# Optimization experiments

Measured on AMD Instinct MI355X. Metric: run time of the kernel, lower is better.

## Reference

```python
import jax, jax.numpy as jnp
import numpy as np

N_NODES = 100000
N_EDGES = 1600000
K = 10          # APPNP propagation steps
ALPHA = 0.1     # teleport probability


def appnp_propagate(src, dst, h):
    """DGL APPNPConv (eval mode, no edge dropout): symmetric-normalized
    k-step personalized-pagerank propagation over the edge list."""
    n = h.shape[0]
    deg = jax.ops.segment_sum(jnp.ones_like(dst, dtype=h.dtype), dst, num_segments=n)
    norm = jnp.clip(deg, 1.0, None) ** -0.5  # [N]
    h0 = h
    for _ in range(K):
        msg = (h * norm[:, None])[src]                      # [E, D] gather
        agg = jax.ops.segment_sum(msg, dst, num_segments=n) # [N, D] scatter-add
        h = (1.0 - ALPHA) * agg * norm[:, None] + ALPHA * h0
    return h


def setup_inputs() -> dict:
    key = jax.random.key(0)
    ks = jax.random.split(key, 7)
    input_dim, hidden, classes = 256, 48, 16
    features = jax.random.normal(ks[0], (N_NODES, input_dim), dtype=jnp.float32)
    src = jax.random.randint(ks[1], (N_EDGES,), 0, N_NODES, dtype=jnp.int32)
    dst = jax.random.randint(ks[2], (N_EDGES,), 0, N_NODES, dtype=jnp.int32)
    # xavier_normal-ish init for fc weights
    W1 = jax.random.normal(ks[3], (hidden, input_dim), dtype=jnp.float32) * (2.0 / (hidden + input_dim)) ** 0.5
    b1 = jnp.zeros((hidden,), dtype=jnp.float32)
    W2 = jax.random.normal(ks[4], (classes, hidden), dtype=jnp.float32) * (2.0 / (classes + hidden)) ** 0.5
    b2 = jnp.zeros((classes,), dtype=jnp.float32)
    return {"features": features, "src": src, "dst": dst,
            "W1": W1, "b1": b1, "W2": W2, "b2": b2}


def reference(features, src, dst, W1, b1, W2, b2):
    # fc1
    h = features @ W1.T + b1              # [N, hidden]
    # layer1: APPNP propagation
    x = appnp_propagate(src, dst, h)
    # fc2 + elu
    x = jax.nn.elu(x @ W2.T + b2)         # [N, classes]
    # layer2: APPNP propagation
    x = appnp_propagate(src, dst, x)
    return jax.nn.elu(x)
```

## Files before the change

### kernel.cpp

```cpp
#include <hip/hip_runtime.h>
#include <hip/hip_fp16.h>
#include <math.h>

#define IN_DIM 256
#define HID 48
#define CLS 16
#define K_STEPS 10
#define ALPHA 0.1f


__global__ void zero_int_kernel(int* __restrict__ p, int n) {
    int i = blockIdx.x * blockDim.x + threadIdx.x;
    if (i < n) p[i] = 0;
}

__global__ void hist_kernel(const int* __restrict__ dst, int* __restrict__ deg, int nE) {
    int i = blockIdx.x * blockDim.x + threadIdx.x;
    if (i < nE) atomicAdd(&deg[dst[i]], 1);
}

__global__ void norm_kernel(const int* __restrict__ deg, float* __restrict__ nrm, int n) {
    int i = blockIdx.x * blockDim.x + threadIdx.x;
    if (i < n) nrm[i] = rsqrtf(fmaxf((float)deg[i], 1.0f));
}


__global__ __launch_bounds__(256) void scan1_kernel(const int* __restrict__ deg,
                                                    int* __restrict__ bsum, int n) {
    __shared__ int ls[256];
    int t = threadIdx.x;
    int base = blockIdx.x * 1024 + t * 4;
    int s = 0;
    if (base + 3 < n) {
        int4 d = *(const int4*)(deg + base);
        s = d.x + d.y + d.z + d.w;
    } else {
        for (int i = 0; i < 4; i++) if (base + i < n) s += deg[base + i];
    }
    ls[t] = s; __syncthreads();
    for (int o = 128; o > 0; o >>= 1) {
        if (t < o) ls[t] += ls[t + o];
        __syncthreads();
    }
    if (t == 0) bsum[blockIdx.x] = ls[0];
}

__global__ void scan2_kernel(int* __restrict__ bsum, int* __restrict__ off, int nb, int n) {
    if (threadIdx.x == 0 && blockIdx.x == 0) {
        int run = 0;
        for (int i = 0; i < nb; i++) { int t = bsum[i]; bsum[i] = run; run += t; }
        off[n] = run;
    }
}

__global__ __launch_bounds__(256) void scan3_kernel(const int* __restrict__ deg,
                                                    const int* __restrict__ bsum,
                                                    int* __restrict__ off,
                                                    int* __restrict__ cursor, int n) {
    __shared__ int ts[256];
    int t = threadIdx.x;
    int base = blockIdx.x * 1024 + t * 4;
    int d0 = 0, d1 = 0, d2 = 0, d3 = 0;
    if (base + 3 < n) {
        int4 d = *(const int4*)(deg + base);
        d0 = d.x; d1 = d.y; d2 = d.z; d3 = d.w;
    } else {
        if (base     < n) d0 = deg[base];
        if (base + 1 < n) d1 = deg[base + 1];
        if (base + 2 < n) d2 = deg[base + 2];
        if (base + 3 < n) d3 = deg[base + 3];
    }
    int s = d0 + d1 + d2 + d3;
    ts[t] = s; __syncthreads();
    for (int o = 1; o < 256; o <<= 1) {
        int v = (t >= o) ? ts[t - o] : 0;
        __syncthreads();
        ts[t] += v;
        __syncthreads();
    }
    int ex = ts[t] - s + bsum[blockIdx.x];
    int p0 = ex, p1 = ex + d0, p2 = p1 + d1, p3 = p2 + d2;
    if (base     < n) { off[base]     = p0; cursor[base]     = p0; }
    if (base + 1 < n) { off[base + 1] = p1; cursor[base + 1] = p1; }
    if (base + 2 < n) { off[base + 2] = p2; cursor[base + 2] = p2; }
    if (base + 3 < n) { off[base + 3] = p3; cursor[base + 3] = p3; }
}

__global__ void fill_kernel(const int* __restrict__ src, const int* __restrict__ dst,
                            int* __restrict__ cursor, int* __restrict__ csrc, int nE) {
    int e = blockIdx.x * blockDim.x + threadIdx.x;
    if (e >= nE) return;
    int p = atomicAdd(&cursor[dst[e]], 1);
    csrc[p] = src[e];
}


__global__ __launch_bounds__(256) void wc_kernel(
    const float* __restrict__ W1, const float* __restrict__ W2,
    const float* __restrict__ b1, float* __restrict__ Wc, float* __restrict__ bc)
{
    int c = blockIdx.x;
    int k = threadIdx.x;
    float acc = 0.0f;
    #pragma unroll
    for (int j = 0; j < HID; j++)
        acc = fmaf(W2[c * HID + j], W1[j * IN_DIM + k], acc);
    Wc[c * IN_DIM + k] = acc;
    if (k == 0) {
        float b = 0.0f;
        for (int j = 0; j < HID; j++) b = fmaf(W2[c * HID + j], b1[j], b);
        bc[c] = b;
    }
}


#define BM 128
#define BK 16
__global__ __launch_bounds__(256) void fcz_kernel(
    const float* __restrict__ X, const float* __restrict__ Wc,
    const float* __restrict__ bc, const float* __restrict__ nrm,
    float* __restrict__ z0, __half* __restrict__ A, int n)
{
    __shared__ float Xs[BK][BM + 1];
    __shared__ float Ws[BK][CLS];
    const int t = threadIdx.x;
    const int tx = t & 31;
    const int ty = t >> 5;
    const int mbase = blockIdx.x * BM;
    float acc[4][2] = {{0}};

    for (int k0 = 0; k0 < IN_DIM; k0 += BK) {
        #pragma unroll
        for (int c0 = 0; c0 < 2; c0++) {
            int c = t + c0 * 256;
            int m = c >> 2, kc = (c & 3) << 2;
            int gm = mbase + m;
            float4 xv = make_float4(0.f, 0.f, 0.f, 0.f);
            if (gm < n) xv = *(const float4*)(X + (size_t)gm * IN_DIM + k0 + kc);
            Xs[kc + 0][m] = xv.x; Xs[kc + 1][m] = xv.y;
            Xs[kc + 2][m] = xv.z; Xs[kc + 3][m] = xv.w;
        }
        if (t < 64) {
            int j = t >> 2, kc = (t & 3) << 2;
            float4 wv = *(const float4*)(Wc + (size_t)j * IN_DIM + k0 + kc);
            Ws[kc + 0][j] = wv.x; Ws[kc + 1][j] = wv.y;
            Ws[kc + 2][j] = wv.z; Ws[kc + 3][j] = wv.w;
        }
        __syncthreads();
        #pragma unroll
        for (int k = 0; k < BK; k++) {
            float a[4], b[2];
            #pragma unroll
            for (int im = 0; im < 4; im++) a[im] = Xs[k][tx + 32 * im];
            #pragma unroll
            for (int jn = 0; jn < 2; jn++) b[jn] = Ws[k][ty * 2 + jn];
            #pragma unroll
            for (int im = 0; im < 4; im++)
                #pragma unroll
                for (int jn = 0; jn < 2; jn++)
                    acc[im][jn] = fmaf(a[im], b[jn], acc[im][jn]);
        }
        __syncthreads();
    }

    #pragma unroll
    for (int im = 0; im < 4; im++) {
        int m = mbase + tx + 32 * im;
        if (m < n) {
            float nv = nrm[m];
            float r0 = acc[im][0] + bc[ty * 2 + 0];
            float r1 = acc[im][1] + bc[ty * 2 + 1];
            size_t idx = (size_t)m * CLS + ty * 2;
            z0[idx] = r0;
            z0[idx + 1] = r1;
            ((__half2*)A)[(size_t)m * 8 + ty] = __floats2half2_rn(r0 * nv, r1 * nv);
        }
    }
}


struct __align__(8) half4 { __half2 a, b; };

__device__ __forceinline__ void hacc(float4& acc, half4 w) {
    float2 lo = __half22float2(w.a);
    float2 hi = __half22float2(w.b);
    acc.x += lo.x; acc.y += lo.y; acc.z += hi.x; acc.w += hi.y;
}
__device__ __forceinline__ float eluf(float x) {
    return x > 0.0f ? x : expm1f(x);
}

template<int MODE>
__global__ __launch_bounds__(256) void gatherh_kernel(
    const int* __restrict__ off, const int* __restrict__ csrc,
    const half4* __restrict__ A, const float4* __restrict__ tele,
    const float* __restrict__ nrm, const float4* __restrict__ b2v,
    half4* __restrict__ outp, float4* __restrict__ x0out,
    float4* __restrict__ outf, int n)
{
    const int v = blockIdx.x * 64 + threadIdx.y;
    if (v >= n) return;
    const int lane = threadIdx.x;

    const int s = off[v], e = off[v + 1];
    float4 a0 = make_float4(0.f, 0.f, 0.f, 0.f), a1 = a0;
    int i = s;
    for (; i + 3 < e; i += 4) {
        int u0 = csrc[i], u1 = csrc[i + 1], u2 = csrc[i + 2], u3 = csrc[i + 3];
        half4 w0 = A[(size_t)u0 * 4 + lane];
        half4 w1 = A[(size_t)u1 * 4 + lane];
        half4 w2 = A[(size_t)u2 * 4 + lane];
        half4 w3 = A[(size_t)u3 * 4 + lane];
        hacc(a0, w0); hacc(a1, w1); hacc(a0, w2); hacc(a1, w3);
    }
    for (; i < e; i++) hacc(a0, A[(size_t)csrc[i] * 4 + lane]);
    a0.x += a1.x; a0.y += a1.y; a0.z += a1.z; a0.w += a1.w;

    float nv = nrm[v];
    size_t o = (size_t)v * 4 + lane;
    float4 hv = tele[o];
    float4 r;
    r.x = (1.0f - ALPHA) * a0.x * nv + ALPHA * hv.x;
    r.y = (1.0f - ALPHA) * a0.y * nv + ALPHA * hv.y;
    r.z = (1.0f - ALPHA) * a0.z * nv + ALPHA * hv.z;
    r.w = (1.0f - ALPHA) * a0.w * nv + ALPHA * hv.w;

    if (MODE == 0) {
        half4 w;
        w.a = __floats2half2_rn(r.x * nv, r.y * nv);
        w.b = __floats2half2_rn(r.z * nv, r.w * nv);
        outp[o] = w;
    } else if (MODE == 1) {
        float4 b = b2v[lane];
        float4 x;
        x.x = eluf(r.x + b.x); x.y = eluf(r.y + b.y);
        x.z = eluf(r.z + b.z); x.w = eluf(r.w + b.w);
        x0out[o] = x;
        half4 w;
        w.a = __floats2half2_rn(x.x * nv, x.y * nv);
        w.b = __floats2half2_rn(x.z * nv, x.w * nv);
        outp[o] = w;
    } else {
        outf[o] = make_float4(eluf(r.x), eluf(r.y), eluf(r.z), eluf(r.w));
    }
}


extern "C" void kernel_launch(void* const* d_in, const int* in_sizes, int n_in,
                              void* d_out, int out_size, void* d_ws, size_t ws_size,
                              hipStream_t stream)
{
    const float* features = (const float*)d_in[0];
    const int*   src      = (const int*)d_in[1];
    const int*   dst      = (const int*)d_in[2];
    const float* W1       = (const float*)d_in[3];
    const float* b1       = (const float*)d_in[4];
    const float* W2       = (const float*)d_in[5];
    const float* b2       = (const float*)d_in[6];
    float* out = (float*)d_out;

    const int n  = in_sizes[0] / IN_DIM;
    const int nE = in_sizes[1];

    float* ws   = (float*)d_ws;
    float* nrm  = ws;
    float* z0   = nrm + n;
    float* x0   = z0 + (size_t)CLS * n;
    float* Wc   = x0 + (size_t)CLS * n;
    float* bc   = Wc + CLS * IN_DIM;
    __half* PH  = (__half*)(bc + 16);
    __half* QH  = PH + (size_t)CLS * n;
    int*   deg    = (int*)(QH + (size_t)CLS * n);
    int*   off    = deg + n;
    int*   cursor = off + n + 4;
    int*   bsum   = cursor + n;
    int*   csrc   = bsum + 1024;

    const int B = 256;
    const int nb = (n + 1023) / 1024;

    zero_int_kernel<<<(n + B - 1) / B, B, 0, stream>>>(deg, n);
    hist_kernel<<<(nE + B - 1) / B, B, 0, stream>>>(dst, deg, nE);
    norm_kernel<<<(n + B - 1) / B, B, 0, stream>>>(deg, nrm, n);
    scan1_kernel<<<nb, 256, 0, stream>>>(deg, bsum, n);
    scan2_kernel<<<1, 64, 0, stream>>>(bsum, off, nb, n);
    scan3_kernel<<<nb, 256, 0, stream>>>(deg, bsum, off, cursor, n);
    fill_kernel<<<(nE + B - 1) / B, B, 0, stream>>>(src, dst, cursor, csrc, nE);

    wc_kernel<<<CLS, 256, 0, stream>>>(W1, W2, b1, Wc, bc);
    fcz_kernel<<<(n + BM - 1) / BM, 256, 0, stream>>>(features, Wc, bc, nrm, z0, PH, n);

    dim3 gblk(4, 64);
    int ggrid = (n + 63) / 64;

    __half* pa = PH; __half* pb = QH;
    for (int k = 0; k < K_STEPS; k++) {
        if (k < K_STEPS - 1)
            gatherh_kernel<0><<<ggrid, gblk, 0, stream>>>(
                off, csrc, (const half4*)pa, (const float4*)z0, nrm,
                nullptr, (half4*)pb, nullptr, nullptr, n);
        else
            gatherh_kernel<1><<<ggrid, gblk, 0, stream>>>(
                off, csrc, (const half4*)pa, (const float4*)z0, nrm,
                (const float4*)b2, (half4*)pb, (float4*)x0, nullptr, n);
        __half* t = pa; pa = pb; pb = t;
    }

    for (int k = 0; k < K_STEPS; k++) {
        if (k < K_STEPS - 1)
            gatherh_kernel<0><<<ggrid, gblk, 0, stream>>>(
                off, csrc, (const half4*)pa, (const float4*)x0, nrm,
                nullptr, (half4*)pb, nullptr, nullptr, n);
        else
            gatherh_kernel<2><<<ggrid, gblk, 0, stream>>>(
                off, csrc, (const half4*)pa, (const float4*)x0, nrm,
                nullptr, nullptr, nullptr, (float4*)out, n);
        __half* t = pa; pa = pb; pb = t;
    }
}
```

Measured before the change: 610.6 us.

## Bucket edges by destination before CSR fill and use 2-lane 16-byte gathers

CSR construction now runs a two-pass bucket sort of the edge list by destination range (histogram, scan, split into a temporary buffer) before the per-node atomic fill. This localizes the cursor atomics and csrc writes. The propagation kernel now gives each node 2 lanes that each load 16 bytes (8 halves) instead of 4 lanes loading 8 bytes. Neighbor indices are loaded as int4 and exchanged between lanes with shuffles to get more loads in flight. The temporary edge buffer reuses the z0 workspace before fcz overwrites it, which adds several kernels and relies on that ordering.

After: 734.2 us. +20.2%, slower.

```diff
diff --git a/kernel.cpp b/kernel.cpp
--- a/kernel.cpp
+++ b/kernel.cpp
@@ -7,6 +7,10 @@
 #define CLS 16
 #define K_STEPS 10
 #define ALPHA 0.1f
+
+#define NBUC 256
+#define NSPLIT 64
+#define BSHIFT 9
 
 
 __global__ void zero_int_kernel(int* __restrict__ p, int n) {
@@ -86,12 +90,66 @@
     if (base + 3 < n) { off[base + 3] = p3; cursor[base + 3] = p3; }
 }
 
-__global__ void fill_kernel(const int* __restrict__ src, const int* __restrict__ dst,
-                            int* __restrict__ cursor, int* __restrict__ csrc, int nE) {
-    int e = blockIdx.x * blockDim.x + threadIdx.x;
-    if (e >= nE) return;
-    int p = atomicAdd(&cursor[dst[e]], 1);
-    csrc[p] = src[e];
+__global__ __launch_bounds__(256) void bhist_kernel(const int* __restrict__ dst,
+                                                    int* __restrict__ mtx, int nE) {
+    __shared__ int cnt[NBUC];
+    int wg = blockIdx.x;
+    for (int i = threadIdx.x; i < NBUC; i += 256) cnt[i] = 0;
+    __syncthreads();
+    int lo = (int)((long long)nE * wg / NSPLIT);
+    int hi = (int)((long long)nE * (wg + 1) / NSPLIT);
+    for (int i = lo + threadIdx.x; i < hi; i += 256)
+        atomicAdd(&cnt[dst[i] >> BSHIFT], 1);
+    __syncthreads();
+    for (int b = threadIdx.x; b < NBUC; b += 256) mtx[b * NSPLIT + wg] = cnt[b];
+}
+
+__global__ __launch_bounds__(NBUC) void bscan_kernel(int* __restrict__ mtx) {
+    __shared__ int ts[NBUC];
+    int b = threadIdx.x;
+    int base_i = b * NSPLIT;
+    int s = 0;
+    for (int w = 0; w < NSPLIT; w++) s += mtx[base_i + w];
+    ts[b] = s; __syncthreads();
+    for (int o = 1; o < NBUC; o <<= 1) {
+        int v = (b >= o) ? ts[b - o] : 0;
+        __syncthreads();
+        ts[b] += v;
+        __syncthreads();
+    }
+    int run = ts[b] - s;
+    for (int w = 0; w < NSPLIT; w++) { int t = mtx[base_i + w]; mtx[base_i + w] = run; run += t; }
+}
+
+__global__ __launch_bounds__(256) void msplit_kernel(const int* __restrict__ src,
+                                                     const int* __restrict__ dst,
+                                                     const int* __restrict__ mtx,
+                                                     int2* __restrict__ ebuf, int nE) {
+    __shared__ int cur[NBUC];
+    int wg = blockIdx.x;
+    for (int b = threadIdx.x; b < NBUC; b += 256) cur[b] = mtx[b * NSPLIT + wg];
+    __syncthreads();
+    int lo = (int)((long long)nE * wg / NSPLIT);
+    int hi = (int)((long long)nE * (wg + 1) / NSPLIT);
+    for (int i = lo + threadIdx.x; i < hi; i += 256) {
+        int d = dst[i];
+        int p = atomicAdd(&cur[d >> BSHIFT], 1);
+        ebuf[p] = make_int2(d, src[i]);
+    }
+}
+
+__global__ __launch_bounds__(256) void ffill_kernel(const int2* __restrict__ ebuf,
+                                                    int* __restrict__ cursor,
+                                                    int* __restrict__ csrc, int nE) {
+    int nwg = gridDim.x;
+    int wg = (blockIdx.x % 8) * (nwg / 8) + blockIdx.x / 8;
+    int lo = (int)((long long)nE * wg / nwg);
+    int hi = (int)((long long)nE * (wg + 1) / nwg);
+    for (int i = lo + threadIdx.x; i < hi; i += 256) {
+        int2 e = ebuf[i];
+        int p = atomicAdd(&cursor[e.x], 1);
+        csrc[p] = e.y;
+    }
 }
 
 
@@ -179,69 +237,103 @@
 }
 
 
-struct __align__(8) half4 { __half2 a, b; };
-
-__device__ __forceinline__ void hacc(float4& acc, half4 w) {
-    float2 lo = __half22float2(w.a);
-    float2 hi = __half22float2(w.b);
-    acc.x += lo.x; acc.y += lo.y; acc.z += hi.x; acc.w += hi.y;
-}
 __device__ __forceinline__ float eluf(float x) {
     return x > 0.0f ? x : expm1f(x);
 }
 
+__device__ __forceinline__ void hacc8(float4& x, float4& y, float4 raw) {
+    __half2* h = reinterpret_cast<__half2*>(&raw);
+    float2 f0 = __half22float2(h[0]);
+    float2 f1 = __half22float2(h[1]);
+    float2 f2 = __half22float2(h[2]);
+    float2 f3 = __half22float2(h[3]);
+    x.x += f0.x; x.y += f0.y; x.z += f1.x; x.w += f1.y;
+    y.x += f2.x; y.y += f2.y; y.z += f3.x; y.w += f3.y;
+}
+
 template<int MODE>
-__global__ __launch_bounds__(256) void gatherh_kernel(
+__global__ __launch_bounds__(256) void gather2_kernel(
     const int* __restrict__ off, const int* __restrict__ csrc,
-    const half4* __restrict__ A, const float4* __restrict__ tele,
-    const float* __restrict__ nrm, const float4* __restrict__ b2v,
-    half4* __restrict__ outp, float4* __restrict__ x0out,
+    const float4* __restrict__ A,
+    const float4* __restrict__ tele,
+    const float* __restrict__ nrm, const float* __restrict__ b2,
+    float4* __restrict__ outpH, float4* __restrict__ x0out,
     float4* __restrict__ outf, int n)
 {
-    const int v = blockIdx.x * 64 + threadIdx.y;
+    const int v = blockIdx.x * 128 + (threadIdx.x >> 1);
     if (v >= n) return;
-    const int lane = threadIdx.x;
+    const int lane = threadIdx.x & 1;
 
     const int s = off[v], e = off[v + 1];
-    float4 a0 = make_float4(0.f, 0.f, 0.f, 0.f), a1 = a0;
+    float4 a0 = make_float4(0.f,0.f,0.f,0.f), a1 = a0, c0 = a0, c1 = a0;
     int i = s;
-    for (; i + 3 < e; i += 4) {
-        int u0 = csrc[i], u1 = csrc[i + 1], u2 = csrc[i + 2], u3 = csrc[i + 3];
-        half4 w0 = A[(size_t)u0 * 4 + lane];
-        half4 w1 = A[(size_t)u1 * 4 + lane];
-        half4 w2 = A[(size_t)u2 * 4 + lane];
-        half4 w3 = A[(size_t)u3 * 4 + lane];
-        hacc(a0, w0); hacc(a1, w1); hacc(a0, w2); hacc(a1, w3);
-    }
-    for (; i < e; i++) hacc(a0, A[(size_t)csrc[i] * 4 + lane]);
-    a0.x += a1.x; a0.y += a1.y; a0.z += a1.z; a0.w += a1.w;
-
-    float nv = nrm[v];
-    size_t o = (size_t)v * 4 + lane;
-    float4 hv = tele[o];
-    float4 r;
-    r.x = (1.0f - ALPHA) * a0.x * nv + ALPHA * hv.x;
-    r.y = (1.0f - ALPHA) * a0.y * nv + ALPHA * hv.y;
-    r.z = (1.0f - ALPHA) * a0.z * nv + ALPHA * hv.z;
-    r.w = (1.0f - ALPHA) * a0.w * nv + ALPHA * hv.w;
+    for (; i < e && (i & 3); i++)
+        hacc8(a0, a1, A[(size_t)csrc[i] * 2 + lane]);
+    for (; i + 8 <= e; i += 8) {
+        int4 me = *(const int4*)(csrc + i + 4 * lane);
+        int4 ot;
+        ot.x = __shfl_xor(me.x, 1); ot.y = __shfl_xor(me.y, 1);
+        ot.z = __shfl_xor(me.z, 1); ot.w = __shfl_xor(me.w, 1);
+        float4 r0 = A[(size_t)me.x * 2 + lane];
+        float4 r1 = A[(size_t)me.y * 2 + lane];
+        float4 r2 = A[(size_t)me.z * 2 + lane];
+        float4 r3 = A[(size_t)me.w * 2 + lane];
+        float4 r4 = A[(size_t)ot.x * 2 + lane];
+        float4 r5 = A[(size_t)ot.y * 2 + lane];
+        float4 r6 = A[(size_t)ot.z * 2 + lane];
+        float4 r7 = A[(size_t)ot.w * 2 + lane];
+        hacc8(a0, a1, r0); hacc8(c0, c1, r1);
+        hacc8(a0, a1, r2); hacc8(c0, c1, r3);
+        hacc8(a0, a1, r4); hacc8(c0, c1, r5);
+        hacc8(a0, a1, r6); hacc8(c0, c1, r7);
+    }
+    for (; i < e; i++)
+        hacc8(a0, a1, A[(size_t)csrc[i] * 2 + lane]);
+    a0.x += c0.x; a0.y += c0.y; a0.z += c0.z; a0.w += c0.w;
+    a1.x += c1.x; a1.y += c1.y; a1.z += c1.z; a1.w += c1.w;
+
+    const float nv = nrm[v];
+    const size_t ro = (size_t)v * 4 + 2 * lane;
+    float4 h0 = tele[ro], h1 = tele[ro + 1];
+    float4 r0, r1;
+    r0.x = (1.0f - ALPHA) * a0.x * nv + ALPHA * h0.x;
+    r0.y = (1.0f - ALPHA) * a0.y * nv + ALPHA * h0.y;
+    r0.z = (1.0f - ALPHA) * a0.z * nv + ALPHA * h0.z;
+    r0.w = (1.0f - ALPHA) * a0.w * nv + ALPHA * h0.w;
+    r1.x = (1.0f - ALPHA) * a1.x * nv + ALPHA * h1.x;
+    r1.y = (1.0f - ALPHA) * a1.y * nv + ALPHA * h1.y;
+    r1.z = (1.0f - ALPHA) * a1.z * nv + ALPHA * h1.z;
+    r1.w = (1.0f - ALPHA) * a1.w * nv + ALPHA * h1.w;
 
     if (MODE == 0) {
-        half4 w;
-        w.a = __floats2half2_rn(r.x * nv, r.y * nv);
-        w.b = __floats2half2_rn(r.z * nv, r.w * nv);
-        outp[o] = w;
+        float4 w;
+        __half2* wh = reinterpret_cast<__half2*>(&w);
+        wh[0] = __floats2half2_rn(r0.x * nv, r0.y * nv);
+        wh[1] = __floats2half2_rn(r0.z * nv, r0.w * nv);
+        wh[2] = __floats2half2_rn(r1.x * nv, r1.y * nv);
+        wh[3] = __floats2half2_rn(r1.z * nv, r1.w * nv);
+        outpH[(size_t)v * 2 + lane] = w;
     } else if (MODE == 1) {
-        float4 b = b2v[lane];
-        float4 x;
-        x.x = eluf(r.x + b.x); x.y = eluf(r.y + b.y);
-        x.z = eluf(r.z + b.z); x.w = eluf(r.w + b.w);
-        x0out[o] = x;
-        half4 w;
-        w.a = __floats2half2_rn(x.x * nv, x.y * nv);
-        w.b = __floats2half2_rn(x.z * nv, x.w * nv);
-        outp[o] = w;
+        const float4* b2v = (const float4*)b2;
+        float4 bb0 = b2v[2 * lane], bb1 = b2v[2 * lane + 1];
+        float4 x0_, x1_;
+        x0_.x = eluf(r0.x + bb0.x); x0_.y = eluf(r0.y + bb0.y);
+        x0_.z = eluf(r0.z + bb0.z); x0_.w = eluf(r0.w + bb0.w);
+        x1_.x = eluf(r1.x + bb1.x); x1_.y = eluf(r1.y + bb1.y);
+        x1_.z = eluf(r1.z + bb1.z); x1_.w = eluf(r1.w + bb1.w);
+        x0out[ro] = x0_; x0out[ro + 1] = x1_;
+        float4 w;
+        __half2* wh = reinterpret_cast<__half2*>(&w);
+        wh[0] = __floats2half2_rn(x0_.x * nv, x0_.y * nv);
+        wh[1] = __floats2half2_rn(x0_.z * nv, x0_.w * nv);
+        wh[2] = __floats2half2_rn(x1_.x * nv, x1_.y * nv);
+        wh[3] = __floats2half2_rn(x1_.z * nv, x1_.w * nv);
+        outpH[(size_t)v * 2 + lane] = w;
     } else {
-        outf[o] = make_float4(eluf(r.x), eluf(r.y), eluf(r.z), eluf(r.w));
+        float4 o0, o1;
+        o0.x = eluf(r0.x); o0.y = eluf(r0.y); o0.z = eluf(r0.z); o0.w = eluf(r0.w);
+        o1.x = eluf(r1.x); o1.y = eluf(r1.y); o1.z = eluf(r1.z); o1.w = eluf(r1.w);
+        outf[ro] = o0; outf[ro + 1] = o1;
     }
 }
 
@@ -275,6 +367,8 @@
     int*   cursor = off + n + 4;
     int*   bsum   = cursor + n;
     int*   csrc   = bsum + 1024;
+    int*   mtx    = csrc + nE;
+    int2*  ebuf   = (int2*)z0;
 
     const int B = 256;
     const int nb = (n + 1023) / 1024;
@@ -285,36 +379,39 @@
     scan1_kernel<<<nb, 256, 0, stream>>>(deg, bsum, n);
     scan2_kernel<<<1, 64, 0, stream>>>(bsum, off, nb, n);
     scan3_kernel<<<nb, 256, 0, stream>>>(deg, bsum, off, cursor, n);
-    fill_kernel<<<(nE + B - 1) / B, B, 0, stream>>>(src, dst, cursor, csrc, nE);
+
+    bhist_kernel<<<NSPLIT, 256, 0, stream>>>(dst, mtx, nE);
+    bscan_kernel<<<1, NBUC, 0, stream>>>(mtx);
+    msplit_kernel<<<NSPLIT, 256, 0, stream>>>(src, dst, mtx, ebuf, nE);
+    ffill_kernel<<<256, 256, 0, stream>>>(ebuf, cursor, csrc, nE);
 
     wc_kernel<<<CLS, 256, 0, stream>>>(W1, W2, b1, Wc, bc);
     fcz_kernel<<<(n + BM - 1) / BM, 256, 0, stream>>>(features, Wc, bc, nrm, z0, PH, n);
 
-    dim3 gblk(4, 64);
-    int ggrid = (n + 63) / 64;
+    int ggrid = (n + 127) / 128;
 
     __half* pa = PH; __half* pb = QH;
     for (int k = 0; k < K_STEPS; k++) {
         if (k < K_STEPS - 1)
-            gatherh_kernel<0><<<ggrid, gblk, 0, stream>>>(
-                off, csrc, (const half4*)pa, (const float4*)z0, nrm,
-                nullptr, (half4*)pb, nullptr, nullptr, n);
+            gather2_kernel<0><<<ggrid, 256, 0, stream>>>(
+                off, csrc, (const float4*)pa, (const float4*)z0, nrm, nullptr,
+                (float4*)pb, nullptr, nullptr, n);
         else
-            gatherh_kernel<1><<<ggrid, gblk, 0, stream>>>(
-                off, csrc, (const half4*)pa, (const float4*)z0, nrm,
-                (const float4*)b2, (half4*)pb, (float4*)x0, nullptr, n);
+            gather2_kernel<1><<<ggrid, 256, 0, stream>>>(
+                off, csrc, (const float4*)pa, (const float4*)z0, nrm, b2,
+                (float4*)pb, (float4*)x0, nullptr, n);
         __half* t = pa; pa = pb; pb = t;
     }
 
     for (int k = 0; k < K_STEPS; k++) {
         if (k < K_STEPS - 1)
-            gatherh_kernel<0><<<ggrid, gblk, 0, stream>>>(
-                off, csrc, (const half4*)pa, (const float4*)x0, nrm,
-                nullptr, (half4*)pb, nullptr, nullptr, n);
+            gather2_kernel<0><<<ggrid, 256, 0, stream>>>(
+                off, csrc, (const float4*)pa, (const float4*)x0, nrm, nullptr,
+                (float4*)pb, nullptr, nullptr, n);
         else
-            gatherh_kernel<2><<<ggrid, gblk, 0, stream>>>(
-                off, csrc, (const half4*)pa, (const float4*)x0, nrm,
-                nullptr, nullptr, nullptr, (float4*)out, n);
+            gather2_kernel<2><<<ggrid, 256, 0, stream>>>(
+                off, csrc, (const float4*)pa, (const float4*)x0, nrm, nullptr,
+                nullptr, nullptr, (float4*)out, n);
         __half* t = pa; pa = pb; pb = t;
     }
 }
```
